# Kernel tuning notes

Hardware: AMD Instinct MI355X
Metric: run time of the kernel (lower is better)

Reference implementation:

```python
import jax, jax.numpy as jnp
import numpy as np

B, L, C, H, W = 4, 8, 32, 128, 256
M1, M2 = 32, 32  # spectral modes


def setup_inputs() -> dict:
    key = jax.random.key(0)
    k1, k2, k3, k4, k5, k6 = jax.random.split(key, 6)
    scale = 1.0 / (C * C)
    return {
        "x": jax.random.normal(k1, (B, L, C, H, W), dtype=jnp.float32),
        "k": jax.random.normal(k2, (C, H, W), dtype=jnp.float32),
        "w1r": scale * jax.random.normal(k3, (C, C, M1, M2), dtype=jnp.float32),
        "w1i": scale * jax.random.normal(k4, (C, C, M1, M2), dtype=jnp.float32),
        "w2r": scale * jax.random.normal(k5, (C, C, M1, M2), dtype=jnp.float32),
        "w2i": scale * jax.random.normal(k6, (C, C, M1, M2), dtype=jnp.float32),
    }


def reference(x, k, w1r, w1i, w2r, w2i):
    # x: [B, L, C, H, W] real; k: [C, H, W] conv kernel (broadcast over B*L).
    b, l, c, h, w = x.shape
    # --- FlashFFTConvInterface fallback path: circular conv via rfft2.
    # H, W are already 2/3/5-smooth (next_fast_len is identity -> no padding).
    u = x.reshape(b * l, c, h, w)
    u_f = jnp.fft.rfft2(u)                     # [B*L, C, H, W//2+1] complex
    k_f = jnp.fft.rfft2(k)                     # [C, H, W//2+1], broadcasts
    y = jnp.fft.irfft2(u_f * k_f, s=(h, w)).reshape(b, l, c, h, w)

    # --- SpectralConv2d: per-mode channel mixing in frequency domain.
    x_f = jnp.fft.rfft2(y)                     # [B, L, C, H, Wf] complex
    wf = x_f.shape[-1]
    w1 = (w1r + 1j * w1i).astype(x_f.dtype)
    w2 = (w2r + 1j * w2i).astype(x_f.dtype)
    m1 = min(h, M1)
    m2 = min(wf, M2)
    co = w1.shape[1]
    top = jnp.einsum('blcij,coij->bloij', x_f[:, :, :, :m1, :m2], w1[:, :, :m1, :m2])
    out_f = jnp.zeros((b, l, co, h, wf), dtype=x_f.dtype)
    out_f = out_f.at[:, :, :, :m1, :m2].set(top)
    if h > 1 and (h > M1 or wf > M2):
        bot = jnp.einsum('blcij,coij->bloij', x_f[:, :, :, h - m1:, :m2], w2[:, :, :m1, :m2])
        out_f = out_f.at[:, :, :, h - m1:, :m2].set(bot)
    return jnp.fft.irfft2(out_f, s=(h, w))    # [B, L, Co, H, W] real
```

## Files before the change

### kernel.cpp

```cpp
#include <hip/hip_runtime.h>
#include <math.h>

#define Hn 128
#define Wn 256
#define PLANE (Hn*Wn)

#define OFF_TQC 0u
#define OFF_TQS 2048u
#define OFF_TP  4096u
#define OFF_KM  16384u
#define OFF_XM  147456u
#define OFF_B   4341760u
#define OFF_RK  12730368u

__global__ __launch_bounds__(256) void build_tables(float* __restrict__ ws) {
  int tid = blockIdx.x * 256 + threadIdx.x;
  const double PI2 = 6.283185307179586476925286766559;
  if (tid < 512) {
    int j = tid >> 4, xi = tid & 15;
    float cc[4], ss[4];
#pragma unroll
    for (int m = 0; m < 4; m++) {
      int x = xi * 4 + m;
      double ang = PI2 * (double)((j * x) & 255) / 256.0;
      cc[m] = (float)cos(ang); ss[m] = (float)sin(ang);
    }
    ((float4*)(ws + OFF_TQC))[tid] = make_float4(cc[0], cc[1], cc[2], cc[3]);
    ((float4*)(ws + OFF_TQS))[tid] = make_float4(ss[0], ss[1], ss[2], ss[3]);
  }
  if (tid < 2048) {
    int p = tid >> 6, y2 = tid & 63;
    double a0 = PI2 * (double)((p * (2 * y2)) & 127) / 128.0;
    double a1 = PI2 * (double)((p * (2 * y2 + 1)) & 127) / 128.0;
    ((float4*)(ws + OFF_TP))[tid] =
        make_float4((float)cos(a0), (float)sin(a0), (float)cos(a1), (float)sin(a1));
  }
}

__device__ __forceinline__ float rot_re(int m, float Sr, float Si) {
  return (m == 0) ? Sr : (m == 1) ? Si : (m == 2) ? -Sr : -Si;
}
__device__ __forceinline__ float rot_im(int m, float Sr, float Si) {
  return (m == 0) ? Si : (m == 1) ? -Sr : (m == 2) ? -Si : Sr;
}

__global__ __launch_bounds__(256) void fwd_rows(const float* __restrict__ src,
                                                float2* __restrict__ R,
                                                const float* __restrict__ ws) {
  int plane = blockIdx.x >> 2, chunk = blockIdx.x & 3;
  __shared__ float4 Us[2048];
  __shared__ float4 Tc[544], Ts[544];
  int t = threadIdx.x;
  const float4* src4 = (const float4*)src;
  size_t sb = (size_t)plane * 8192 + (size_t)chunk * 2048;
#pragma unroll
  for (int k = 0; k < 8; k++) {
    int idx = t + 256 * k;
    int row = idx >> 6, col4 = idx & 63;
    Us[row * 64 + (col4 ^ ((row >> 1) & 15))] = src4[sb + idx];
  }
  const float4* gTc = (const float4*)(ws + OFF_TQC);
  const float4* gTs = (const float4*)(ws + OFF_TQS);
#pragma unroll
  for (int k = 0; k < 2; k++) {
    int idx = t + 256 * k;
    Tc[(idx >> 4) * 17 + (idx & 15)] = gTc[idx];
    Ts[(idx >> 4) * 17 + (idx & 15)] = gTs[idx];
  }
  __syncthreads();
  int jg = t & 15, yg = t >> 4;
  float ar[2][2][4], ai[2][2][4];
#pragma unroll
  for (int a = 0; a < 2; a++)
#pragma unroll
    for (int b = 0; b < 2; b++)
#pragma unroll
      for (int q = 0; q < 4; q++) { ar[a][b][q] = 0.f; ai[a][b][q] = 0.f; }
  for (int xb = 0; xb < 16; xb++) {
    float4 c0 = Tc[jg * 17 + xb],        s0 = Ts[jg * 17 + xb];
    float4 c1 = Tc[(jg + 16) * 17 + xb], s1 = Ts[(jg + 16) * 17 + xb];
#pragma unroll
    for (int ky = 0; ky < 2; ky++) {
      int y = yg * 2 + ky;
      int sw = (y >> 1) & 15;
      int base = y * 64;
#pragma unroll
      for (int q = 0; q < 4; q++) {
        float4 u4 = Us[base + ((q * 16 + xb) ^ sw)];
        ar[0][ky][q] += u4.x * c0.x + u4.y * c0.y + u4.z * c0.z + u4.w * c0.w;
        ai[0][ky][q] -= u4.x * s0.x + u4.y * s0.y + u4.z * s0.z + u4.w * s0.w;
        ar[1][ky][q] += u4.x * c1.x + u4.y * c1.y + u4.z * c1.z + u4.w * c1.w;
        ai[1][ky][q] -= u4.x * s1.x + u4.y * s1.y + u4.z * s1.z + u4.w * s1.w;
      }
    }
  }
#pragma unroll
  for (int jj = 0; jj < 2; jj++) {
    int j = jg + 16 * jj;
    int m1 = j & 3, m2 = (2 * j) & 3, m3 = (3 * j) & 3;
#pragma unroll
    for (int ky = 0; ky < 2; ky++) {
      int y = chunk * 32 + yg * 2 + ky;
      float re = ar[jj][ky][0], im = ai[jj][ky][0];
      re += rot_re(m1, ar[jj][ky][1], ai[jj][ky][1]);
      im += rot_im(m1, ar[jj][ky][1], ai[jj][ky][1]);
      re += rot_re(m2, ar[jj][ky][2], ai[jj][ky][2]);
      im += rot_im(m2, ar[jj][ky][2], ai[jj][ky][2]);
      re += rot_re(m3, ar[jj][ky][3], ai[jj][ky][3]);
      im += rot_im(m3, ar[jj][ky][3], ai[jj][ky][3]);
      R[((size_t)plane * 128 + y) * 32 + j] = make_float2(re, im);
    }
  }
}

__global__ __launch_bounds__(256) void fwd_cols(const float2* __restrict__ Rg,
                                                float2* __restrict__ dst,
                                                const float* __restrict__ ws) {
  int plane = blockIdx.x;
  __shared__ float4 Rs4[2048];
  __shared__ float4 TPs[2048];
  float2* Rs = (float2*)Rs4;
  int t = threadIdx.x;
  const float4* in4 = (const float4*)(Rg + (size_t)plane * 4096);
#pragma unroll
  for (int k = 0; k < 8; k++) Rs4[t + 256 * k] = in4[t + 256 * k];
  const float4* gTP = (const float4*)(ws + OFF_TP);
#pragma unroll
  for (int k = 0; k < 8; k++) TPs[t + 256 * k] = gTP[t + 256 * k];
  __syncthreads();
  int j = t & 31, pg = t >> 5;
  float Are[4], Aim[4], Bre[4], Bim[4];
#pragma unroll
  for (int m = 0; m < 4; m++) { Are[m] = Aim[m] = Bre[m] = Bim[m] = 0.f; }
  for (int it = 0; it < 32; it++) {
#pragma unroll
    for (int h = 0; h < 2; h++) {
      int y2 = 2 * it + h;
      float sg = (h == 0) ? 1.f : -1.f;
      float2 r0 = Rs[(2 * y2) * 32 + j];
      float2 r1 = Rs[(2 * y2 + 1) * 32 + j];
#pragma unroll
      for (int m = 0; m < 4; m++) {
        int p = pg + 8 * m;
        float4 tw = TPs[p * 64 + y2];
        float P0 = r0.x * tw.x + r0.y * tw.y;
        float Q0 = r0.y * tw.x - r0.x * tw.y;
        float P1 = r1.x * tw.z + r1.y * tw.w;
        float Q1 = r1.y * tw.z - r1.x * tw.w;
        Are[m] += P0 + P1;
        Aim[m] += Q0 + Q1;
        Bre[m] += sg * (P0 - Q1);
        Bim[m] += sg * (Q0 + P1);
      }
    }
  }
  size_t ob = (size_t)plane * 2048;
#pragma unroll
  for (int m = 0; m < 4; m++) {
    int p = pg + 8 * m;
    dst[ob + p * 32 + j] = make_float2(Are[m], Aim[m]);
    dst[ob + (32 + p) * 32 + j] = make_float2(Bre[m], Bim[m]);
  }
}

__global__ __launch_bounds__(256) void wk_build(const float* __restrict__ w1r,
                                                const float* __restrict__ w1i,
                                                const float* __restrict__ w2r,
                                                const float* __restrict__ w2i,
                                                float2* __restrict__ wk,
                                                const float2* __restrict__ km) {
  int e0 = blockIdx.x * 256 + threadIdx.x;
#pragma unroll
  for (int k = 0; k < 4; k++) {
    int e = e0 + k * 524288;
    int o = e & 31, c = (e >> 5) & 31, j = (e >> 10) & 31, i64 = e >> 15;
    int r = (i64 < 32) ? i64 : i64 - 32;
    const float* wr = (i64 < 32) ? w1r : w2r;
    const float* wi = (i64 < 32) ? w1i : w2i;
    int widx = ((c * 32 + o) * 32 + r) * 32 + j;
    float wrv = wr[widx], wiv = wi[widx];
    float2 kv = km[(size_t)c * 2048 + i64 * 32 + j];
    wk[e] = make_float2(kv.x * wrv - kv.y * wiv, kv.x * wiv + kv.y * wrv);
  }
}

__global__ __launch_bounds__(256) void mix_modes(float2* __restrict__ xm,
                                                 const float2* __restrict__ wk) {
  int bid = blockIdx.x;
  int mode = (bid & 7) * 256 + (bid >> 3);
  __shared__ float4 Xs4[512], Ws4[512];
  float2* Xs = (float2*)Xs4;
  float2* Wsl = (float2*)Ws4;
  int t = threadIdx.x;
#pragma unroll
  for (int k = 0; k < 4; k++) {
    int p = t + 256 * k;
    Xs[p] = xm[(size_t)p * 2048 + mode];
  }
  const float4* wk4 = (const float4*)(wk + (size_t)mode * 1024);
#pragma unroll
  for (int k = 0; k < 2; k++) Ws4[t + 256 * k] = wk4[t + 256 * k];
  __syncthreads();
  int o = t & 31, bg = t >> 5;
  float orr[4], oii[4];
#pragma unroll
  for (int m = 0; m < 4; m++) { orr[m] = 0.f; oii[m] = 0.f; }
  for (int c2 = 0; c2 < 16; c2++) {
    float2 w0 = Wsl[(2 * c2) * 32 + o];
    float2 w1 = Wsl[(2 * c2 + 1) * 32 + o];
#pragma unroll
    for (int m = 0; m < 4; m++) {
      float4 xv = *(const float4*)&Xs[(bg * 4 + m) * 32 + 2 * c2];
      orr[m] += xv.x * w0.x - xv.y * w0.y + xv.z * w1.x - xv.w * w1.y;
      oii[m] += xv.x * w0.y + xv.y * w0.x + xv.z * w1.y + xv.w * w1.x;
    }
  }
#pragma unroll
  for (int m = 0; m < 4; m++)
    xm[(size_t)((bg * 4 + m) * 32 + o) * 2048 + mode] = make_float2(orr[m], oii[m]);
}

__global__ __launch_bounds__(256) void inv_rows(const float2* __restrict__ om,
                                                float2* __restrict__ G,
                                                const float* __restrict__ ws) {
  int plane = blockIdx.x;
  __shared__ float4 Os4[1024];
  __shared__ float4 TPs[2048];
  float2* Os = (float2*)Os4;
  int t = threadIdx.x;
  const float4* in4 = (const float4*)(om + (size_t)plane * 2048);
#pragma unroll
  for (int k = 0; k < 4; k++) Os4[t + 256 * k] = in4[t + 256 * k];
  const float4* gTP = (const float4*)(ws + OFF_TP);
#pragma unroll
  for (int k = 0; k < 8; k++) TPs[t + 256 * k] = gTP[t + 256 * k];
  __syncthreads();
  int j = t & 31, yg = t >> 5;
  float gr[16], gi[16];
#pragma unroll
  for (int k = 0; k < 16; k++) { gr[k] = 0.f; gi[k] = 0.f; }
  for (int p = 0; p < 32; p++) {
    float2 A = Os[p * 32 + j];
    float2 B = Os[(32 + p) * 32 + j];
#pragma unroll
    for (int mp = 0; mp < 8; mp++) {
      int y2 = yg * 8 + mp;
      float4 tw = TPs[p * 64 + y2];
      float sg = ((mp & 1) == 0) ? 1.f : -1.f;
      float Sr = A.x + sg * B.x, Si = A.y + sg * B.y;
      gr[2 * mp]     += Sr * tw.x - Si * tw.y;
      gi[2 * mp]     += Sr * tw.y + Si * tw.x;
      float Tr = A.x + sg * B.y, Ti = A.y - sg * B.x;
      gr[2 * mp + 1] += Tr * tw.z - Ti * tw.w;
      gi[2 * mp + 1] += Tr * tw.w + Ti * tw.z;
    }
  }
  const float inv = 1.0f / 32768.0f;
  size_t gb = (size_t)plane * 128;
#pragma unroll
  for (int mm = 0; mm < 16; mm++) {
    int y = yg * 16 + mm;
    float sr = (j == 0) ? gr[mm] * inv : 2.f * inv * gr[mm];
    float si = (j == 0) ? 0.f : 2.f * inv * gi[mm];
    G[(gb + y) * 32 + j] = make_float2(sr, si);
  }
}

__global__ __launch_bounds__(256) void inv_cols(const float2* __restrict__ G,
                                                float* __restrict__ out,
                                                const float* __restrict__ ws) {
  int plane = blockIdx.x >> 2, chunk = blockIdx.x & 3;
  __shared__ float2 Gs[32 * 33];
  __shared__ float4 Tc[544], Ts[544];
  int t = threadIdx.x;
  const float2* in = G + (size_t)plane * 4096 + (size_t)chunk * 1024;
#pragma unroll
  for (int k = 0; k < 4; k++) {
    int idx = t + 256 * k;
    Gs[(idx >> 5) * 33 + (idx & 31)] = in[idx];
  }
  const float4* gTc = (const float4*)(ws + OFF_TQC);
  const float4* gTs = (const float4*)(ws + OFF_TQS);
#pragma unroll
  for (int k = 0; k < 2; k++) {
    int idx = t + 256 * k;
    Tc[(idx >> 4) * 17 + (idx & 15)] = gTc[idx];
    Ts[(idx >> 4) * 17 + (idx & 15)] = gTs[idx];
  }
  __syncthreads();
  int xi = t & 15, yg = t >> 4;
  float4 acc[2][4];
#pragma unroll
  for (int ky = 0; ky < 2; ky++)
#pragma unroll
    for (int q = 0; q < 4; q++) acc[ky][q] = make_float4(0.f, 0.f, 0.f, 0.f);
  for (int jjb = 0; jjb < 8; jjb++) {
#pragma unroll
    for (int jjo = 0; jjo < 4; jjo++) {
      int jj = jjb * 4 + jjo;
      float4 c4 = Tc[jj * 17 + xi];
      float4 s4 = Ts[jj * 17 + xi];
#pragma unroll
      for (int ky = 0; ky < 2; ky++) {
        float2 g = Gs[(yg * 2 + ky) * 33 + jj];
        float4 P, Q;
        P.x = g.x * c4.x - g.y * s4.x;  P.y = g.x * c4.y - g.y * s4.y;
        P.z = g.x * c4.z - g.y * s4.z;  P.w = g.x * c4.w - g.y * s4.w;
        Q.x = g.x * s4.x + g.y * c4.x;  Q.y = g.x * s4.y + g.y * c4.y;
        Q.z = g.x * s4.z + g.y * c4.z;  Q.w = g.x * s4.w + g.y * c4.w;
#pragma unroll
        for (int q = 0; q < 4; q++) {
          int m = (jjo * q) & 3;
          if (m == 0) {
            acc[ky][q].x += P.x; acc[ky][q].y += P.y; acc[ky][q].z += P.z; acc[ky][q].w += P.w;
          } else if (m == 1) {
            acc[ky][q].x -= Q.x; acc[ky][q].y -= Q.y; acc[ky][q].z -= Q.z; acc[ky][q].w -= Q.w;
          } else if (m == 2) {
            acc[ky][q].x -= P.x; acc[ky][q].y -= P.y; acc[ky][q].z -= P.z; acc[ky][q].w -= P.w;
          } else {
            acc[ky][q].x += Q.x; acc[ky][q].y += Q.y; acc[ky][q].z += Q.z; acc[ky][q].w += Q.w;
          }
        }
      }
    }
  }
  float* outp = out + (size_t)plane * PLANE + (size_t)chunk * 32 * Wn;
#pragma unroll
  for (int ky = 0; ky < 2; ky++) {
    int y = yg * 2 + ky;
#pragma unroll
    for (int q = 0; q < 4; q++)
      *(float4*)(outp + y * Wn + q * 64 + xi * 4) = acc[ky][q];
  }
}

extern "C" void kernel_launch(void* const* d_in, const int* in_sizes, int n_in,
                              void* d_out, int out_size, void* d_ws, size_t ws_size,
                              hipStream_t stream) {
  (void)in_sizes; (void)n_in; (void)out_size; (void)ws_size;
  const float* x   = (const float*)d_in[0];
  const float* kk  = (const float*)d_in[1];
  const float* w1r = (const float*)d_in[2];
  const float* w1i = (const float*)d_in[3];
  const float* w2r = (const float*)d_in[4];
  const float* w2i = (const float*)d_in[5];
  float*  ws   = (float*)d_ws;
  float*  out  = (float*)d_out;
  float2* km2  = (float2*)(ws + OFF_KM);
  float2* xm2  = (float2*)(ws + OFF_XM);
  float2* bx   = (float2*)(ws + OFF_B);
  float2* rk   = (float2*)(ws + OFF_RK);

  build_tables<<<8, 256, 0, stream>>>(ws);
  fwd_rows<<<4096, 256, 0, stream>>>(x, bx, ws);
  fwd_rows<<<128, 256, 0, stream>>>(kk, rk, ws);
  fwd_cols<<<1024, 256, 0, stream>>>(bx, xm2, ws);
  fwd_cols<<<32, 256, 0, stream>>>(rk, km2, ws);
  wk_build<<<2048, 256, 0, stream>>>(w1r, w1i, w2r, w2i, bx, km2);
  mix_modes<<<2048, 256, 0, stream>>>(xm2, bx);
  inv_rows<<<1024, 256, 0, stream>>>(xm2, bx, ws);
  inv_cols<<<4096, 256, 0, stream>>>(bx, out, ws);
}
```

Baseline: 447.8 us.

## Use even/odd real-input symmetry to halve row DFT work in fwd_rows

The row DFT kernel now folds each real row into even (x[n]+x[N-n]) and odd (x[n]-x[N-n]) parts in shared memory, then computes the cosine and sine sums over only half the samples, using quarter-period table symmetry to pick cos/sin tables per output frequency. This is meant to roughly halve the multiply-add count of the direct DFT. It adds an extra shared-memory pass with two barriers, a padded shared layout, and a launch_bounds occupancy hint of 3 blocks per CU. The index bookkeeping for the Nyquist and zero terms is intricate and could introduce subtle errors.

Result: faster. 426.4 us (-4.8%).

```diff
diff --git a/kernel.cpp b/kernel.cpp
--- a/kernel.cpp
+++ b/kernel.cpp
@@ -37,18 +37,11 @@
   }
 }
 
-__device__ __forceinline__ float rot_re(int m, float Sr, float Si) {
-  return (m == 0) ? Sr : (m == 1) ? Si : (m == 2) ? -Sr : -Si;
-}
-__device__ __forceinline__ float rot_im(int m, float Sr, float Si) {
-  return (m == 0) ? Si : (m == 1) ? -Sr : (m == 2) ? -Si : Sr;
-}
-
-__global__ __launch_bounds__(256) void fwd_rows(const float* __restrict__ src,
-                                                float2* __restrict__ R,
-                                                const float* __restrict__ ws) {
+__global__ __launch_bounds__(256, 3) void fwd_rows(const float* __restrict__ src,
+                                                   float2* __restrict__ R,
+                                                   const float* __restrict__ ws) {
   int plane = blockIdx.x >> 2, chunk = blockIdx.x & 3;
-  __shared__ float4 Us[2048];
+  __shared__ __align__(16) float Sd[32 * 260];
   __shared__ float4 Tc[544], Ts[544];
   int t = threadIdx.x;
   const float4* src4 = (const float4*)src;
@@ -56,8 +49,9 @@
 #pragma unroll
   for (int k = 0; k < 8; k++) {
     int idx = t + 256 * k;
-    int row = idx >> 6, col4 = idx & 63;
-    Us[row * 64 + (col4 ^ ((row >> 1) & 15))] = src4[sb + idx];
+    int row = idx >> 6, c4 = idx & 63;
+    int sws = (row >> 1) & 15;
+    *(float4*)&Sd[row * 260 + ((c4 ^ sws) << 2)] = src4[sb + idx];
   }
   const float4* gTc = (const float4*)(ws + OFF_TQC);
   const float4* gTs = (const float4*)(ws + OFF_TQS);
@@ -68,46 +62,104 @@
     Ts[(idx >> 4) * 17 + (idx & 15)] = gTs[idx];
   }
   __syncthreads();
+  float eA[4][4], oA[4][4];
+#pragma unroll
+  for (int uu = 0; uu < 4; uu++) {
+    int unit = uu * 256 + t;
+    int y = unit >> 5, xb = unit & 31;
+    int sws = (y >> 1) & 15;
+    const float* rowp = &Sd[y * 260];
+    float4 A = *(const float4*)&rowp[(xb ^ sws) << 2];
+    float Av[4] = {A.x, A.y, A.z, A.w};
+    float M[4];
+#pragma unroll
+    for (int kk = 0; kk < 4; kk++) {
+      int xm = 256 - 4 * xb - kk;
+      int xmc = (xm > 255) ? 255 : xm;
+      int c4m = xmc >> 2, e = xmc & 3;
+      float v = rowp[((c4m ^ sws) << 2) + e];
+      M[kk] = (xm > 255) ? 0.f : v;
+    }
+#pragma unroll
+    for (int kk = 0; kk < 4; kk++) {
+      eA[uu][kk] = Av[kk] + M[kk];
+      oA[uu][kk] = Av[kk] - M[kk];
+    }
+    if (xb == 0) {
+      oA[uu][0] = rowp[(32 ^ sws) << 2];
+    }
+  }
+  __syncthreads();
+#pragma unroll
+  for (int uu = 0; uu < 4; uu++) {
+    int unit = uu * 256 + t;
+    int y = unit >> 5, xb = unit & 31;
+    int sws = (y >> 1) & 15;
+    float* rowp = &Sd[y * 260];
+    *(float4*)&rowp[(xb ^ sws) << 2] =
+        make_float4(eA[uu][0], eA[uu][1], eA[uu][2], eA[uu][3]);
+    *(float4*)&rowp[((32 + xb) ^ sws) << 2] =
+        make_float4(oA[uu][0], oA[uu][1], oA[uu][2], oA[uu][3]);
+  }
+  __syncthreads();
   int jg = t & 15, yg = t >> 4;
-  float ar[2][2][4], ai[2][2][4];
+  int jm = jg & 3;
+  const float4* pC0 = &Tc[jg * 17];
+  const float4* pS0 = &Ts[jg * 17];
+  const float4* pC1 = &Tc[(jg + 16) * 17];
+  const float4* pS1 = &Ts[(jg + 16) * 17];
+  const float4* p2_0 = (jm & 1) ? pS0 : pC0;
+  const float4* p4_0 = (jm & 1) ? pC0 : pS0;
+  const float4* p2_1 = (jm & 1) ? pS1 : pC1;
+  const float4* p4_1 = (jm & 1) ? pC1 : pS1;
+  float sa = (jm == 0 || jm == 3) ? 1.f : -1.f;
+  float sb_ = (jm < 2) ? 1.f : -1.f;
+  float pm = (jg & 1) ? -1.f : 1.f;
+  int sw = yg & 15;
+  const float* row0 = &Sd[(2 * yg) * 260];
+  const float* row1 = &Sd[(2 * yg + 1) * 260];
+  float d1[2][2], d2[2][2], d3[2][2], d4[2][2];
 #pragma unroll
   for (int a = 0; a < 2; a++)
 #pragma unroll
-    for (int b = 0; b < 2; b++)
-#pragma unroll
-      for (int q = 0; q < 4; q++) { ar[a][b][q] = 0.f; ai[a][b][q] = 0.f; }
+    for (int b = 0; b < 2; b++) { d1[a][b] = 0.f; d2[a][b] = 0.f; d3[a][b] = 0.f; d4[a][b] = 0.f; }
+#define DOT4(a, b) (a.x * b.x + a.y * b.y + a.z * b.z + a.w * b.w)
+#pragma unroll 4
   for (int xb = 0; xb < 16; xb++) {
-    float4 c0 = Tc[jg * 17 + xb],        s0 = Ts[jg * 17 + xb];
-    float4 c1 = Tc[(jg + 16) * 17 + xb], s1 = Ts[(jg + 16) * 17 + xb];
-#pragma unroll
-    for (int ky = 0; ky < 2; ky++) {
-      int y = yg * 2 + ky;
-      int sw = (y >> 1) & 15;
-      int base = y * 64;
-#pragma unroll
-      for (int q = 0; q < 4; q++) {
-        float4 u4 = Us[base + ((q * 16 + xb) ^ sw)];
-        ar[0][ky][q] += u4.x * c0.x + u4.y * c0.y + u4.z * c0.z + u4.w * c0.w;
-        ai[0][ky][q] -= u4.x * s0.x + u4.y * s0.y + u4.z * s0.z + u4.w * s0.w;
-        ar[1][ky][q] += u4.x * c1.x + u4.y * c1.y + u4.z * c1.z + u4.w * c1.w;
-        ai[1][ky][q] -= u4.x * s1.x + u4.y * s1.y + u4.z * s1.z + u4.w * s1.w;
-      }
-    }
-  }
+    int off = (xb ^ sw) << 2;
+    float4 e0y0 = *(const float4*)&row0[off];
+    float4 e1y0 = *(const float4*)&row0[off + 64];
+    float4 o0y0 = *(const float4*)&row0[off + 128];
+    float4 o1y0 = *(const float4*)&row0[off + 192];
+    float4 e0y1 = *(const float4*)&row1[off];
+    float4 e1y1 = *(const float4*)&row1[off + 64];
+    float4 o0y1 = *(const float4*)&row1[off + 128];
+    float4 o1y1 = *(const float4*)&row1[off + 192];
+    float4 c0 = pC0[xb], s0 = pS0[xb];
+    float4 t20 = p2_0[xb], t40 = p4_0[xb];
+    float4 c1 = pC1[xb], s1 = pS1[xb];
+    float4 t21 = p2_1[xb], t41 = p4_1[xb];
+    d1[0][0] += DOT4(e0y0, c0);  d1[0][1] += DOT4(e0y1, c0);
+    d1[1][0] += DOT4(e0y0, c1);  d1[1][1] += DOT4(e0y1, c1);
+    d2[0][0] += DOT4(e1y0, t20); d2[0][1] += DOT4(e1y1, t20);
+    d2[1][0] += DOT4(e1y0, t21); d2[1][1] += DOT4(e1y1, t21);
+    d3[0][0] += DOT4(o0y0, s0);  d3[0][1] += DOT4(o0y1, s0);
+    d3[1][0] += DOT4(o0y0, s1);  d3[1][1] += DOT4(o0y1, s1);
+    d4[0][0] += DOT4(o1y0, t40); d4[0][1] += DOT4(o1y1, t40);
+    d4[1][0] += DOT4(o1y0, t41); d4[1][1] += DOT4(o1y1, t41);
+  }
+#undef DOT4
+  float u128_0 = row0[128 + 4 * sw];
+  float u128_1 = row1[128 + 4 * sw];
 #pragma unroll
   for (int jj = 0; jj < 2; jj++) {
     int j = jg + 16 * jj;
-    int m1 = j & 3, m2 = (2 * j) & 3, m3 = (3 * j) & 3;
 #pragma unroll
     for (int ky = 0; ky < 2; ky++) {
       int y = chunk * 32 + yg * 2 + ky;
-      float re = ar[jj][ky][0], im = ai[jj][ky][0];
-      re += rot_re(m1, ar[jj][ky][1], ai[jj][ky][1]);
-      im += rot_im(m1, ar[jj][ky][1], ai[jj][ky][1]);
-      re += rot_re(m2, ar[jj][ky][2], ai[jj][ky][2]);
-      im += rot_im(m2, ar[jj][ky][2], ai[jj][ky][2]);
-      re += rot_re(m3, ar[jj][ky][3], ai[jj][ky][3]);
-      im += rot_im(m3, ar[jj][ky][3], ai[jj][ky][3]);
+      float u128 = ky ? u128_1 : u128_0;
+      float re = d1[jj][ky] + sa * d2[jj][ky] + pm * u128;
+      float im = -(d3[jj][ky] + sb_ * d4[jj][ky]);
       R[((size_t)plane * 128 + y) * 32 + j] = make_float2(re, im);
     }
   }
```
